# Kernel optimization log

Hardware: AMD Instinct MI355X
Metric: run time of the kernel (lower is better)

## Reference

```python
import jax, jax.numpy as jnp
import numpy as np
from functools import partial

N_NODES = 100000
N_EDGES = 3200000
F_IN, H1, H2, C_OUT = 128, 64, 32, 2


def setup_inputs() -> dict:
    key = jax.random.key(0)
    ks = jax.random.split(key, 8)
    x = jax.random.normal(ks[0], (N_NODES, F_IN), dtype=jnp.float32)
    edge_index = jax.random.randint(ks[1], (2, N_EDGES), 0, N_NODES, dtype=jnp.int64)
    def glorot(k, fan_in, fan_out):
        s = jnp.sqrt(6.0 / (fan_in + fan_out))
        return jax.random.uniform(k, (fan_in, fan_out), jnp.float32, -s, s)
    return {
        "x": x,
        "edge_index": edge_index,
        "W1": glorot(ks[2], F_IN, H1), "b1": jnp.zeros((H1,), jnp.float32),
        "W2": glorot(ks[3], H1, H2),   "b2": jnp.zeros((H2,), jnp.float32),
        "W3": glorot(ks[4], H2, C_OUT), "b3": jnp.zeros((C_OUT,), jnp.float32),
    }


def _gcn_norm(edge_index, num_nodes):
    # add self-loops, compute symmetric normalization D^{-1/2} (A+I) D^{-1/2}
    loop = jnp.arange(num_nodes, dtype=edge_index.dtype)
    src = jnp.concatenate([edge_index[0], loop])
    dst = jnp.concatenate([edge_index[1], loop])
    deg = jax.ops.segment_sum(jnp.ones_like(dst, dtype=jnp.float32), dst,
                              num_segments=num_nodes)
    dinv = jax.lax.rsqrt(deg)  # deg >= 1 because of self-loops
    norm = dinv[src] * dinv[dst]  # [E + N]
    return src, dst, norm


def _gcn_conv(x, W, b, src, dst, norm, num_nodes):
    # PyG GCNConv: linear transform, then normalized scatter-aggregate, then bias
    xw = x @ W                                   # [N, F_out]
    msg = xw[src] * norm[:, None]                # [E+N, F_out] gather + scale
    out = jax.ops.segment_sum(msg, dst, num_segments=num_nodes)
    return out + b


def reference(x, edge_index, W1, b1, W2, b2, W3, b3):
    n = x.shape[0]
    src, dst, norm = _gcn_norm(edge_index, n)
    h = jax.nn.relu(_gcn_conv(x, W1, b1, src, dst, norm, n))
    # dropout is identity in eval mode
    h = jax.nn.relu(_gcn_conv(h, W2, b2, src, dst, norm, n))
    h = _gcn_conv(h, W3, b3, src, dst, norm, n)
    return jax.nn.log_softmax(h, axis=1)
```

## Files before the change

kernel.cpp:

```cpp
#include <hip/hip_runtime.h>
#include <hip/hip_bf16.h>
#include <math.h>

constexpr int N = 100000;
constexpr int E = 3200000;
constexpr int FIN = 128, H1 = 64, H2 = 32, COUT = 2;

constexpr int BUK_SHIFT = 6;
constexpr int BUK_NODES = 64;
constexpr int NBUK = (N + BUK_NODES - 1) / BUK_NODES;
constexpr int CAP = 2560;
constexpr int SEG_SHIFT = 14;
constexpr int NSEG = 7;
constexpr int KEYS = BUK_NODES * NSEG;
constexpr int RP_STR = BUK_NODES + 1;

constexpr int MS_TPB = 1024;
constexpr int MS_EPT = 24;
constexpr int CHUNK = MS_TPB * MS_EPT;
constexpr int MS_WGS = (E + CHUNK - 1) / CHUNK;

__global__ void k_initcur(int* __restrict__ gcursor) {
    int i = blockIdx.x * blockDim.x + threadIdx.x;
    if (i < NBUK) gcursor[i] = i * CAP;
}

__global__ __launch_bounds__(MS_TPB)
void k_mslice(const int* __restrict__ src, const int* __restrict__ dst,
              int* __restrict__ gcursor, unsigned* __restrict__ ebuf) {
    __shared__ int cnt[NBUK];
    __shared__ int base[NBUK];
    const int t = threadIdx.x;
    for (int i = t; i < NBUK; i += MS_TPB) cnt[i] = 0;
    __syncthreads();
    const int e0 = blockIdx.x * CHUNK;

    int rb[MS_EPT];
    unsigned rv[MS_EPT];
#pragma unroll
    for (int j = 0; j < MS_EPT; ++j) {
        int e = e0 + j * MS_TPB + t;
        if (e < E) {
            int d = dst[e];
            int b = d >> BUK_SHIFT;
            rb[j] = b;
            rv[j] = (unsigned)src[e] | ((unsigned)(d & (BUK_NODES - 1)) << 17);
            atomicAdd(&cnt[b], 1);
        } else {
            rb[j] = -1; rv[j] = 0;
        }
    }
    __syncthreads();
    for (int i = t; i < NBUK; i += MS_TPB) {
        int c = cnt[i];
        base[i] = c ? atomicAdd(&gcursor[i], c) : 0;
    }
    __syncthreads();
    for (int i = t; i < NBUK; i += MS_TPB) cnt[i] = 0;
    __syncthreads();
#pragma unroll
    for (int j = 0; j < MS_EPT; ++j) {
        int b = rb[j];
        if (b >= 0) {
            int r = atomicAdd(&cnt[b], 1);
            int p = base[b] + r;
            if (p < (b + 1) * CAP) ebuf[p] = rv[j];
        }
    }
}

__global__ __launch_bounds__(256)
void k_build(const int* __restrict__ gcursor, unsigned* __restrict__ ebuf,
             int* __restrict__ rp, float* __restrict__ dinv) {
    __shared__ unsigned ent[CAP];
    __shared__ int cnt[512];
    __shared__ int sa[512];
    __shared__ int sb[512];
    __shared__ int cur[512];
    const int b = blockIdx.x;
    const int t = threadIdx.x;
    int fill = gcursor[b] - b * CAP;
    if (fill > CAP) fill = CAP;
    const int gbase = b * CAP;

    cnt[t] = 0; cnt[t + 256] = 0;
    __syncthreads();
    for (int j = t; j < fill; j += 256) {
        unsigned v = ebuf[gbase + j];
        ent[j] = v;
        int key = (int)(v >> 17) * NSEG + (int)((v & 0x1FFFFu) >> SEG_SHIFT);
        atomicAdd(&cnt[key], 1);
    }
    __syncthreads();
    sa[t] = cnt[t]; sa[t + 256] = cnt[t + 256];
    __syncthreads();
    int* pin = sa; int* pout = sb;
    for (int off = 1; off < 512; off <<= 1) {
        pout[t]       = pin[t]       + ((t >= off)       ? pin[t - off]       : 0);
        pout[t + 256] = pin[t + 256] + ((t + 256 >= off) ? pin[t + 256 - off] : 0);
        __syncthreads();
        int* tmp = pin; pin = pout; pout = tmp;
    }
    {
        int ex0 = pin[t] - cnt[t];
        int ex1 = pin[t + 256] - cnt[t + 256];
        cur[t] = gbase + ex0;
        cur[t + 256] = gbase + ex1;
        if (t < KEYS && (t % NSEG) == 0)
            rp[b * RP_STR + t / NSEG] = gbase + ex0;
        int k2 = t + 256;
        if (k2 < KEYS && (k2 % NSEG) == 0)
            rp[b * RP_STR + k2 / NSEG] = gbase + ex1;
        if (t == 0) rp[b * RP_STR + BUK_NODES] = gbase + fill;
    }
    if (t < BUK_NODES) {
        int deg = 0;
#pragma unroll
        for (int s = 0; s < NSEG; ++s) deg += cnt[t * NSEG + s];
        int node = (b << BUK_SHIFT) + t;
        if (node < N) dinv[node] = rsqrtf((float)deg + 1.0f);
    }
    __syncthreads();
    for (int j = t; j < fill; j += 256) {
        unsigned v = ent[j];
        int key = (int)(v >> 17) * NSEG + (int)((v & 0x1FFFFu) >> SEG_SHIFT);
        int p = atomicAdd(&cur[key], 1);
        ebuf[p] = v & 0x1FFFFu;
    }
}

template<int FI, int FO>
__global__ __launch_bounds__(256)
void k_gemm_tile_bf(const float* __restrict__ h, const float* __restrict__ Wg,
                    const float* __restrict__ dinv, __hip_bfloat16* __restrict__ y) {
    constexpr int TX  = FO / 4;
    constexpr int TY  = 256 / TX;
    constexpr int RPT = 64 / TY;
    constexpr int XS  = 68;
    constexpr int KQ  = FI / 4;

    __shared__ float xsT[FI][XS];

    const int tid = threadIdx.x;
    const int tx = tid % TX;
    const int ty = tid / TX;
    const int row0 = blockIdx.x * 64;

    for (int idx = tid; idx < 64 * KQ; idx += 256) {
        int g   = idx / 8;
        int rlo = idx % 8;
        int k4  = g % KQ;
        int rhi = g / KQ;
        int r   = rlo + 8 * rhi;
        int row = row0 + r;
        float4 v = make_float4(0.f, 0.f, 0.f, 0.f);
        if (row < N) v = *(const float4*)(h + (size_t)row * FI + 4 * k4);
        xsT[4 * k4 + 0][r] = v.x;
        xsT[4 * k4 + 1][r] = v.y;
        xsT[4 * k4 + 2][r] = v.z;
        xsT[4 * k4 + 3][r] = v.w;
    }
    __syncthreads();

    float acc[RPT][4];
#pragma unroll
    for (int i = 0; i < RPT; ++i)
#pragma unroll
        for (int c = 0; c < 4; ++c) acc[i][c] = 0.0f;

#pragma unroll 4
    for (int k = 0; k < FI; ++k) {
        const float4 wv = *(const float4*)(Wg + (size_t)k * FO + 4 * tx);
        float xv[RPT];
        if constexpr (RPT == 4) {
            float4 t = *(const float4*)&xsT[k][4 * ty];
            xv[0] = t.x; xv[1] = t.y; xv[2] = t.z; xv[3] = t.w;
        } else {
            float2 t = *(const float2*)&xsT[k][2 * ty];
            xv[0] = t.x; xv[1] = t.y;
        }
#pragma unroll
        for (int i = 0; i < RPT; ++i) {
            acc[i][0] = fmaf(xv[i], wv.x, acc[i][0]);
            acc[i][1] = fmaf(xv[i], wv.y, acc[i][1]);
            acc[i][2] = fmaf(xv[i], wv.z, acc[i][2]);
            acc[i][3] = fmaf(xv[i], wv.w, acc[i][3]);
        }
    }

#pragma unroll
    for (int i = 0; i < RPT; ++i) {
        int row = row0 + ty * RPT + i;
        if (row >= N) continue;
        float di = dinv[row];
        auto cvt = [](float f) -> unsigned short {
            __hip_bfloat16 b = __float2bfloat16(f);
            return *reinterpret_cast<unsigned short*>(&b);
        };
        ushort4 pk;
        pk.x = cvt(di * acc[i][0]);
        pk.y = cvt(di * acc[i][1]);
        pk.z = cvt(di * acc[i][2]);
        pk.w = cvt(di * acc[i][3]);
        *(ushort4*)&y[(size_t)row * FO + 4 * tx] = pk;
    }
}

template<int FI, int FO, int ROWS>
__global__ __launch_bounds__(FO * ROWS)
void k_gemm_scale(const float* __restrict__ h, const float* __restrict__ W,
                  const float* __restrict__ dinv, float* __restrict__ y) {
    __shared__ float xs[ROWS][FI];
    const int j = threadIdx.x;
    const int r = threadIdx.y;
    const int row0 = blockIdx.x * ROWS;
    const int tid = r * FO + j;
    constexpr int NT = FO * ROWS;
    for (int t = tid; t < ROWS * FI; t += NT) {
        int rr = t / FI, kk = t % FI;
        int row = row0 + rr;
        xs[rr][kk] = (row < N) ? h[(size_t)row * FI + kk] : 0.0f;
    }
    __syncthreads();
    const int row = row0 + r;
    if (row >= N) return;
    float acc = 0.0f;
#pragma unroll
    for (int k = 0; k < FI; ++k)
        acc = fmaf(xs[r][k], W[k * FO + j], acc);
    y[(size_t)row * FO + j] = dinv[row] * acc;
}

template<int F, bool RELU>
__global__ __launch_bounds__(256)
void k_agg_v(const int* __restrict__ rp, const unsigned* __restrict__ csr,
             const __hip_bfloat16* __restrict__ y, const float* __restrict__ dinv,
             const float* __restrict__ b, float* __restrict__ out) {
    constexpr int LPN = F / 8;
    constexpr int NPB = 256 / LPN;
    const int fp = threadIdx.x;
    const int n = blockIdx.x * NPB + threadIdx.y;
    if (n >= N) return;
    const uint4* yq = (const uint4*)y;

    float acc[8];
    auto unpk = [](unsigned w, float& lo, float& hi) {
        lo = __uint_as_float(w << 16);
        hi = __uint_as_float(w & 0xffff0000u);
    };
    auto accum = [&](uint4 v) {
        float l0, h0, l1, h1, l2, h2, l3, h3;
        unpk(v.x, l0, h0); unpk(v.y, l1, h1);
        unpk(v.z, l2, h2); unpk(v.w, l3, h3);
        acc[0] += l0; acc[1] += h0; acc[2] += l1; acc[3] += h1;
        acc[4] += l2; acc[5] += h2; acc[6] += l3; acc[7] += h3;
    };

    {
        uint4 v = yq[(size_t)n * LPN + fp];
        float l0, h0, l1, h1, l2, h2, l3, h3;
        unpk(v.x, l0, h0); unpk(v.y, l1, h1);
        unpk(v.z, l2, h2); unpk(v.w, l3, h3);
        acc[0] = l0; acc[1] = h0; acc[2] = l1; acc[3] = h1;
        acc[4] = l2; acc[5] = h2; acc[6] = l3; acc[7] = h3;
    }

    const int rb = (n >> BUK_SHIFT) * RP_STR + (n & (BUK_NODES - 1));
    int j = rp[rb];
    const int j1 = rp[rb + 1];
    for (; j + 8 <= j1; j += 8) {
        int s0 = (int)csr[j],     s1 = (int)csr[j + 1], s2 = (int)csr[j + 2], s3 = (int)csr[j + 3];
        int s4 = (int)csr[j + 4], s5 = (int)csr[j + 5], s6 = (int)csr[j + 6], s7 = (int)csr[j + 7];
        uint4 v0 = yq[(size_t)s0 * LPN + fp], v1 = yq[(size_t)s1 * LPN + fp];
        uint4 v2 = yq[(size_t)s2 * LPN + fp], v3 = yq[(size_t)s3 * LPN + fp];
        uint4 v4 = yq[(size_t)s4 * LPN + fp], v5 = yq[(size_t)s5 * LPN + fp];
        uint4 v6 = yq[(size_t)s6 * LPN + fp], v7 = yq[(size_t)s7 * LPN + fp];
        accum(v0); accum(v1); accum(v2); accum(v3);
        accum(v4); accum(v5); accum(v6); accum(v7);
    }
    for (; j < j1; ++j) {
        uint4 v = yq[(size_t)(int)csr[j] * LPN + fp];
        accum(v);
    }

    const float di = dinv[n];
    float4 o0, o1;
    o0.x = fmaf(di, acc[0], b[8 * fp + 0]);
    o0.y = fmaf(di, acc[1], b[8 * fp + 1]);
    o0.z = fmaf(di, acc[2], b[8 * fp + 2]);
    o0.w = fmaf(di, acc[3], b[8 * fp + 3]);
    o1.x = fmaf(di, acc[4], b[8 * fp + 4]);
    o1.y = fmaf(di, acc[5], b[8 * fp + 5]);
    o1.z = fmaf(di, acc[6], b[8 * fp + 6]);
    o1.w = fmaf(di, acc[7], b[8 * fp + 7]);
    if (RELU) {
        o0.x = fmaxf(o0.x, 0.f); o0.y = fmaxf(o0.y, 0.f);
        o0.z = fmaxf(o0.z, 0.f); o0.w = fmaxf(o0.w, 0.f);
        o1.x = fmaxf(o1.x, 0.f); o1.y = fmaxf(o1.y, 0.f);
        o1.z = fmaxf(o1.z, 0.f); o1.w = fmaxf(o1.w, 0.f);
    }
    float* op = out + (size_t)n * F + 8 * fp;
    *(float4*)op = o0;
    *(float4*)(op + 4) = o1;
}

__global__ __launch_bounds__(256)
void k_final(const int* __restrict__ rp, const unsigned* __restrict__ csr,
             const float* __restrict__ y, const float* __restrict__ dinv,
             const float* __restrict__ bias, float* __restrict__ out) {
    const int c = threadIdx.x;
    const int n = blockIdx.x * 128 + threadIdx.y;
    float z = 0.0f;
    if (n < N) {
        const int rb = (n >> BUK_SHIFT) * RP_STR + (n & (BUK_NODES - 1));
        int j = rp[rb];
        const int j1 = rp[rb + 1];
        float acc = y[2 * n + c];
        for (; j + 4 <= j1; j += 4) {
            int s0 = (int)csr[j], s1 = (int)csr[j + 1], s2 = (int)csr[j + 2], s3 = (int)csr[j + 3];
            float a0 = y[2 * s0 + c], a1 = y[2 * s1 + c];
            float a2 = y[2 * s2 + c], a3 = y[2 * s3 + c];
            acc += (a0 + a1) + (a2 + a3);
        }
        for (; j < j1; ++j) acc += y[2 * (int)csr[j] + c];
        z = fmaf(dinv[n], acc, bias[c]);
    }
    float zo = __shfl_xor(z, 1);
    if (n < N) {
        float m = fmaxf(z, zo);
        float lse = m + logf(expf(z - m) + expf(zo - m));
        out[2 * n + c] = z - lse;
    }
}

extern "C" void kernel_launch(void* const* d_in, const int* in_sizes, int n_in,
                              void* d_out, int out_size, void* d_ws, size_t ws_size,
                              hipStream_t stream) {
    const float* x   = (const float*)d_in[0];
    const int*   ei  = (const int*)d_in[1];
    const float* W1  = (const float*)d_in[2];
    const float* b1  = (const float*)d_in[3];
    const float* W2  = (const float*)d_in[4];
    const float* b2  = (const float*)d_in[5];
    const float* W3  = (const float*)d_in[6];
    const float* b3  = (const float*)d_in[7];
    float* out = (float*)d_out;

    const int* src = ei;
    const int* dst = ei + E;

    char* p = (char*)d_ws;
    float*    dinv    = (float*)p;    p += (size_t)N * 4;
    int*      gcursor = (int*)p;      p += (size_t)NBUK * 4;
    int*      rp      = (int*)p;      p += (size_t)NBUK * RP_STR * 4;
    unsigned* ebuf    = (unsigned*)p; p += (size_t)NBUK * CAP * 4;
    char*     bufA    = p;            p += (size_t)N * 64 * 4;
    char*     bufB    = p;            p += (size_t)N * 64 * 4;

    __hip_bfloat16* y1 = (__hip_bfloat16*)bufA;
    float*          h1 = (float*)bufB;
    __hip_bfloat16* y2 = (__hip_bfloat16*)bufA;
    float*          h2 = (float*)(bufA + (size_t)N * H2 * 2);
    float*          y3 = (float*)bufB;

    k_initcur<<<(NBUK + 255) / 256, 256, 0, stream>>>(gcursor);
    k_mslice <<<MS_WGS, MS_TPB, 0, stream>>>(src, dst, gcursor, ebuf);
    k_build  <<<NBUK, 256, 0, stream>>>(gcursor, ebuf, rp, dinv);

    k_gemm_tile_bf<FIN, H1><<<(N + 63) / 64, 256, 0, stream>>>(x, W1, dinv, y1);
    k_agg_v<H1, true><<<(N + 31) / 32, dim3(8, 32), 0, stream>>>(rp, ebuf, y1, dinv, b1, h1);

    k_gemm_tile_bf<H1, H2><<<(N + 63) / 64, 256, 0, stream>>>(h1, W2, dinv, y2);
    k_agg_v<H2, true><<<(N + 63) / 64, dim3(4, 64), 0, stream>>>(rp, ebuf, y2, dinv, b2, h2);

    k_gemm_scale<H2, COUT, 128><<<(N + 127) / 128, dim3(COUT, 128), 0, stream>>>(h2, W3, dinv, y3);
    k_final<<<(N + 127) / 128, dim3(2, 128), 0, stream>>>(rp, ebuf, y3, dinv, b3, out);
}
```

Measured before the change: 380.5 us.

## Slice bf16 features into 16-wide planes and aggregate one plane per pass

```diff
diff --git a/kernel.cpp b/kernel.cpp
--- a/kernel.cpp
+++ b/kernel.cpp
@@ -19,6 +19,8 @@
 constexpr int MS_EPT = 24;
 constexpr int CHUNK = MS_TPB * MS_EPT;
 constexpr int MS_WGS = (E + CHUNK - 1) / CHUNK;
+
+typedef float f32x4 __attribute__((ext_vector_type(4)));
 
 __global__ void k_initcur(int* __restrict__ gcursor) {
     int i = blockIdx.x * blockDim.x + threadIdx.x;
@@ -133,6 +135,7 @@
 __global__ __launch_bounds__(256)
 void k_gemm_tile_bf(const float* __restrict__ h, const float* __restrict__ Wg,
                     const float* __restrict__ dinv, __hip_bfloat16* __restrict__ y) {
+    static_assert(FO % 16 == 0, "slice width 16");
     constexpr int TX  = FO / 4;
     constexpr int TY  = 256 / TX;
     constexpr int RPT = 64 / TY;
@@ -188,6 +191,8 @@
         }
     }
 
+    const int p  = (4 * tx) / 16;
+    const int fo = (4 * tx) % 16;
 #pragma unroll
     for (int i = 0; i < RPT; ++i) {
         int row = row0 + ty * RPT + i;
@@ -202,7 +207,7 @@
         pk.y = cvt(di * acc[i][1]);
         pk.z = cvt(di * acc[i][2]);
         pk.w = cvt(di * acc[i][3]);
-        *(ushort4*)&y[(size_t)row * FO + 4 * tx] = pk;
+        *(ushort4*)&y[((size_t)p * N + row) * 16 + fo] = pk;
     }
 }
 
@@ -233,75 +238,86 @@
 
 template<int F, bool RELU>
 __global__ __launch_bounds__(256)
-void k_agg_v(const int* __restrict__ rp, const unsigned* __restrict__ csr,
-             const __hip_bfloat16* __restrict__ y, const float* __restrict__ dinv,
-             const float* __restrict__ b, float* __restrict__ out) {
-    constexpr int LPN = F / 8;
-    constexpr int NPB = 256 / LPN;
+void k_agg_pw(const int* __restrict__ rp, const unsigned* __restrict__ csr,
+              const __hip_bfloat16* __restrict__ y, const float* __restrict__ dinv,
+              const float* __restrict__ b, float* __restrict__ out) {
+    constexpr int NPASS = F / 16;
+    constexpr int QPP   = 2;
+    constexpr int NPB   = 256 / QPP;
     const int fp = threadIdx.x;
     const int n = blockIdx.x * NPB + threadIdx.y;
     if (n >= N) return;
     const uint4* yq = (const uint4*)y;
 
-    float acc[8];
+    const int rb = (n >> BUK_SHIFT) * RP_STR + (n & (BUK_NODES - 1));
+    const int j0 = rp[rb];
+    const int j1 = rp[rb + 1];
+    const float di = dinv[n];
+
     auto unpk = [](unsigned w, float& lo, float& hi) {
         lo = __uint_as_float(w << 16);
         hi = __uint_as_float(w & 0xffff0000u);
     };
-    auto accum = [&](uint4 v) {
-        float l0, h0, l1, h1, l2, h2, l3, h3;
-        unpk(v.x, l0, h0); unpk(v.y, l1, h1);
-        unpk(v.z, l2, h2); unpk(v.w, l3, h3);
-        acc[0] += l0; acc[1] += h0; acc[2] += l1; acc[3] += h1;
-        acc[4] += l2; acc[5] += h2; acc[6] += l3; acc[7] += h3;
-    };
-
-    {
-        uint4 v = yq[(size_t)n * LPN + fp];
-        float l0, h0, l1, h1, l2, h2, l3, h3;
-        unpk(v.x, l0, h0); unpk(v.y, l1, h1);
-        unpk(v.z, l2, h2); unpk(v.w, l3, h3);
-        acc[0] = l0; acc[1] = h0; acc[2] = l1; acc[3] = h1;
-        acc[4] = l2; acc[5] = h2; acc[6] = l3; acc[7] = h3;
-    }
-
-    const int rb = (n >> BUK_SHIFT) * RP_STR + (n & (BUK_NODES - 1));
-    int j = rp[rb];
-    const int j1 = rp[rb + 1];
-    for (; j + 8 <= j1; j += 8) {
-        int s0 = (int)csr[j],     s1 = (int)csr[j + 1], s2 = (int)csr[j + 2], s3 = (int)csr[j + 3];
-        int s4 = (int)csr[j + 4], s5 = (int)csr[j + 5], s6 = (int)csr[j + 6], s7 = (int)csr[j + 7];
-        uint4 v0 = yq[(size_t)s0 * LPN + fp], v1 = yq[(size_t)s1 * LPN + fp];
-        uint4 v2 = yq[(size_t)s2 * LPN + fp], v3 = yq[(size_t)s3 * LPN + fp];
-        uint4 v4 = yq[(size_t)s4 * LPN + fp], v5 = yq[(size_t)s5 * LPN + fp];
-        uint4 v6 = yq[(size_t)s6 * LPN + fp], v7 = yq[(size_t)s7 * LPN + fp];
-        accum(v0); accum(v1); accum(v2); accum(v3);
-        accum(v4); accum(v5); accum(v6); accum(v7);
-    }
-    for (; j < j1; ++j) {
-        uint4 v = yq[(size_t)(int)csr[j] * LPN + fp];
-        accum(v);
-    }
-
-    const float di = dinv[n];
-    float4 o0, o1;
-    o0.x = fmaf(di, acc[0], b[8 * fp + 0]);
-    o0.y = fmaf(di, acc[1], b[8 * fp + 1]);
-    o0.z = fmaf(di, acc[2], b[8 * fp + 2]);
-    o0.w = fmaf(di, acc[3], b[8 * fp + 3]);
-    o1.x = fmaf(di, acc[4], b[8 * fp + 4]);
-    o1.y = fmaf(di, acc[5], b[8 * fp + 5]);
-    o1.z = fmaf(di, acc[6], b[8 * fp + 6]);
-    o1.w = fmaf(di, acc[7], b[8 * fp + 7]);
-    if (RELU) {
-        o0.x = fmaxf(o0.x, 0.f); o0.y = fmaxf(o0.y, 0.f);
-        o0.z = fmaxf(o0.z, 0.f); o0.w = fmaxf(o0.w, 0.f);
-        o1.x = fmaxf(o1.x, 0.f); o1.y = fmaxf(o1.y, 0.f);
-        o1.z = fmaxf(o1.z, 0.f); o1.w = fmaxf(o1.w, 0.f);
-    }
-    float* op = out + (size_t)n * F + 8 * fp;
-    *(float4*)op = o0;
-    *(float4*)(op + 4) = o1;
+
+#pragma unroll 1
+    for (int p = 0; p < NPASS; ++p) {
+        const size_t sbase = (size_t)p * N * QPP + fp;
+        float acc[8];
+        {
+            uint4 v = yq[sbase + (size_t)n * QPP];
+            unpk(v.x, acc[0], acc[1]); unpk(v.y, acc[2], acc[3]);
+            unpk(v.z, acc[4], acc[5]); unpk(v.w, acc[6], acc[7]);
+        }
+        auto accum = [&](uint4 v) {
+            float l0, h0, l1, h1, l2, h2, l3, h3;
+            unpk(v.x, l0, h0); unpk(v.y, l1, h1);
+            unpk(v.z, l2, h2); unpk(v.w, l3, h3);
+            acc[0] += l0; acc[1] += h0; acc[2] += l1; acc[3] += h1;
+            acc[4] += l2; acc[5] += h2; acc[6] += l3; acc[7] += h3;
+        };
+
+        int j = j0;
+        for (; j + 8 <= j1; j += 8) {
+            int s0 = (int)__builtin_nontemporal_load(&csr[j]);
+            int s1 = (int)__builtin_nontemporal_load(&csr[j + 1]);
+            int s2 = (int)__builtin_nontemporal_load(&csr[j + 2]);
+            int s3 = (int)__builtin_nontemporal_load(&csr[j + 3]);
+            int s4 = (int)__builtin_nontemporal_load(&csr[j + 4]);
+            int s5 = (int)__builtin_nontemporal_load(&csr[j + 5]);
+            int s6 = (int)__builtin_nontemporal_load(&csr[j + 6]);
+            int s7 = (int)__builtin_nontemporal_load(&csr[j + 7]);
+            uint4 v0 = yq[sbase + (size_t)s0 * QPP], v1 = yq[sbase + (size_t)s1 * QPP];
+            uint4 v2 = yq[sbase + (size_t)s2 * QPP], v3 = yq[sbase + (size_t)s3 * QPP];
+            uint4 v4 = yq[sbase + (size_t)s4 * QPP], v5 = yq[sbase + (size_t)s5 * QPP];
+            uint4 v6 = yq[sbase + (size_t)s6 * QPP], v7 = yq[sbase + (size_t)s7 * QPP];
+            accum(v0); accum(v1); accum(v2); accum(v3);
+            accum(v4); accum(v5); accum(v6); accum(v7);
+        }
+        for (; j < j1; ++j) {
+            int s = (int)__builtin_nontemporal_load(&csr[j]);
+            accum(yq[sbase + (size_t)s * QPP]);
+        }
+
+        const float* bp = b + p * 16 + 8 * fp;
+        f32x4 o0, o1;
+        o0.x = fmaf(di, acc[0], bp[0]);
+        o0.y = fmaf(di, acc[1], bp[1]);
+        o0.z = fmaf(di, acc[2], bp[2]);
+        o0.w = fmaf(di, acc[3], bp[3]);
+        o1.x = fmaf(di, acc[4], bp[4]);
+        o1.y = fmaf(di, acc[5], bp[5]);
+        o1.z = fmaf(di, acc[6], bp[6]);
+        o1.w = fmaf(di, acc[7], bp[7]);
+        if (RELU) {
+            o0.x = fmaxf(o0.x, 0.f); o0.y = fmaxf(o0.y, 0.f);
+            o0.z = fmaxf(o0.z, 0.f); o0.w = fmaxf(o0.w, 0.f);
+            o1.x = fmaxf(o1.x, 0.f); o1.y = fmaxf(o1.y, 0.f);
+            o1.z = fmaxf(o1.z, 0.f); o1.w = fmaxf(o1.w, 0.f);
+        }
+        float* op = out + (size_t)n * F + p * 16 + 8 * fp;
+        __builtin_nontemporal_store(o0, (f32x4*)op);
+        __builtin_nontemporal_store(o1, (f32x4*)(op + 4));
+    }
 }
 
 __global__ __launch_bounds__(256)
@@ -368,10 +384,10 @@
     k_build  <<<NBUK, 256, 0, stream>>>(gcursor, ebuf, rp, dinv);
 
     k_gemm_tile_bf<FIN, H1><<<(N + 63) / 64, 256, 0, stream>>>(x, W1, dinv, y1);
-    k_agg_v<H1, true><<<(N + 31) / 32, dim3(8, 32), 0, stream>>>(rp, ebuf, y1, dinv, b1, h1);
+    k_agg_pw<H1, true><<<(N + 127) / 128, dim3(2, 128), 0, stream>>>(rp, ebuf, y1, dinv, b1, h1);
 
     k_gemm_tile_bf<H1, H2><<<(N + 63) / 64, 256, 0, stream>>>(h1, W2, dinv, y2);
-    k_agg_v<H2, true><<<(N + 63) / 64, dim3(4, 64), 0, stream>>>(rp, ebuf, y2, dinv, b2, h2);
+    k_agg_pw<H2, true><<<(N + 127) / 128, dim3(2, 128), 0, stream>>>(rp, ebuf, y2, dinv, b2, h2);
 
     k_gemm_scale<H2, COUT, 128><<<(N + 127) / 128, dim3(COUT, 128), 0, stream>>>(h2, W3, dinv, y3);
     k_final<<<(N + 127) / 128, dim3(2, 128), 0, stream>>>(rp, ebuf, y3, dinv, b3, out);
```

New measurement: 520.2 us. 36.7% more time.

## Use split-bf16 MFMA for dense GCN layer GEMMs

Applied to the files above, without the earlier changes.

```diff
diff --git a/kernel.cpp b/kernel.cpp
--- a/kernel.cpp
+++ b/kernel.cpp
@@ -19,6 +19,10 @@
 constexpr int MS_EPT = 24;
 constexpr int CHUNK = MS_TPB * MS_EPT;
 constexpr int MS_WGS = (E + CHUNK - 1) / CHUNK;
+
+typedef float f32x4 __attribute__((ext_vector_type(4)));
+typedef short bf16x8 __attribute__((ext_vector_type(8)));
+typedef short s16x4 __attribute__((ext_vector_type(4)));
 
 __global__ void k_initcur(int* __restrict__ gcursor) {
     int i = blockIdx.x * blockDim.x + threadIdx.x;
@@ -131,78 +135,97 @@
 
 template<int FI, int FO>
 __global__ __launch_bounds__(256)
-void k_gemm_tile_bf(const float* __restrict__ h, const float* __restrict__ Wg,
-                    const float* __restrict__ dinv, __hip_bfloat16* __restrict__ y) {
-    constexpr int TX  = FO / 4;
-    constexpr int TY  = 256 / TX;
-    constexpr int RPT = 64 / TY;
-    constexpr int XS  = 68;
-    constexpr int KQ  = FI / 4;
-
-    __shared__ float xsT[FI][XS];
+void k_gemm_mfma(const float* __restrict__ h, const float* __restrict__ Wg,
+                 const float* __restrict__ dinv, __hip_bfloat16* __restrict__ y) {
+    constexpr int KH  = (FI > 64) ? 64 : FI;
+    constexpr int NPH = FI / KH;
+    constexpr int KP  = KH + 8;
+    constexpr int NCT = FO / 16;
+
+    __shared__ short xh[64 * KP];
+    __shared__ short xl[64 * KP];
+    __shared__ short wh[FO * KP];
+    __shared__ short wl[FO * KP];
 
     const int tid = threadIdx.x;
-    const int tx = tid % TX;
-    const int ty = tid / TX;
+    const int w   = tid >> 6;
+    const int l   = tid & 63;
+    const int lm  = l & 15;
+    const int lg  = l >> 4;
     const int row0 = blockIdx.x * 64;
 
-    for (int idx = tid; idx < 64 * KQ; idx += 256) {
-        int g   = idx / 8;
-        int rlo = idx % 8;
-        int k4  = g % KQ;
-        int rhi = g / KQ;
-        int r   = rlo + 8 * rhi;
-        int row = row0 + r;
-        float4 v = make_float4(0.f, 0.f, 0.f, 0.f);
-        if (row < N) v = *(const float4*)(h + (size_t)row * FI + 4 * k4);
-        xsT[4 * k4 + 0][r] = v.x;
-        xsT[4 * k4 + 1][r] = v.y;
-        xsT[4 * k4 + 2][r] = v.z;
-        xsT[4 * k4 + 3][r] = v.w;
-    }
-    __syncthreads();
-
-    float acc[RPT][4];
-#pragma unroll
-    for (int i = 0; i < RPT; ++i)
-#pragma unroll
-        for (int c = 0; c < 4; ++c) acc[i][c] = 0.0f;
-
-#pragma unroll 4
-    for (int k = 0; k < FI; ++k) {
-        const float4 wv = *(const float4*)(Wg + (size_t)k * FO + 4 * tx);
-        float xv[RPT];
-        if constexpr (RPT == 4) {
-            float4 t = *(const float4*)&xsT[k][4 * ty];
-            xv[0] = t.x; xv[1] = t.y; xv[2] = t.z; xv[3] = t.w;
-        } else {
-            float2 t = *(const float2*)&xsT[k][2 * ty];
-            xv[0] = t.x; xv[1] = t.y;
-        }
-#pragma unroll
-        for (int i = 0; i < RPT; ++i) {
-            acc[i][0] = fmaf(xv[i], wv.x, acc[i][0]);
-            acc[i][1] = fmaf(xv[i], wv.y, acc[i][1]);
-            acc[i][2] = fmaf(xv[i], wv.z, acc[i][2]);
-            acc[i][3] = fmaf(xv[i], wv.w, acc[i][3]);
-        }
-    }
-
-#pragma unroll
-    for (int i = 0; i < RPT; ++i) {
-        int row = row0 + ty * RPT + i;
-        if (row >= N) continue;
-        float di = dinv[row];
-        auto cvt = [](float f) -> unsigned short {
-            __hip_bfloat16 b = __float2bfloat16(f);
-            return *reinterpret_cast<unsigned short*>(&b);
-        };
-        ushort4 pk;
-        pk.x = cvt(di * acc[i][0]);
-        pk.y = cvt(di * acc[i][1]);
-        pk.z = cvt(di * acc[i][2]);
-        pk.w = cvt(di * acc[i][3]);
-        *(ushort4*)&y[(size_t)row * FO + 4 * tx] = pk;
+    auto cvt_hi = [](float f) -> short {
+        __hip_bfloat16 b = __float2bfloat16(f);
+        return *reinterpret_cast<short*>(&b);
+    };
+    auto bf2f = [](short s) -> float {
+        return __uint_as_float(((unsigned)(unsigned short)s) << 16);
+    };
+
+    f32x4 acc[NCT];
+#pragma unroll
+    for (int ct = 0; ct < NCT; ++ct) acc[ct] = f32x4{0.f, 0.f, 0.f, 0.f};
+
+    for (int ph = 0; ph < NPH; ++ph) {
+        if (ph) __syncthreads();
+        for (int idx = tid; idx < 64 * KH / 4; idx += 256) {
+            int r  = idx / (KH / 4);
+            int k4 = idx % (KH / 4);
+            int row = row0 + r;
+            float4 v = make_float4(0.f, 0.f, 0.f, 0.f);
+            if (row < N) v = *(const float4*)(h + (size_t)row * FI + ph * KH + 4 * k4);
+            float vv[4] = {v.x, v.y, v.z, v.w};
+            s16x4 ph4, pl4;
+#pragma unroll
+            for (int i = 0; i < 4; ++i) {
+                short hi = cvt_hi(vv[i]);
+                ph4[i] = hi;
+                pl4[i] = cvt_hi(vv[i] - bf2f(hi));
+            }
+            *(s16x4*)&xh[r * KP + 4 * k4] = ph4;
+            *(s16x4*)&xl[r * KP + 4 * k4] = pl4;
+        }
+        for (int idx = tid; idx < KH * FO; idx += 256) {
+            int k = idx / FO;
+            int c = idx % FO;
+            float wv = Wg[(size_t)(ph * KH + k) * FO + c];
+            short hi = cvt_hi(wv);
+            wh[c * KP + k] = hi;
+            wl[c * KP + k] = cvt_hi(wv - bf2f(hi));
+        }
+        __syncthreads();
+
+#pragma unroll
+        for (int k0 = 0; k0 < KH; k0 += 32) {
+            const int ka = (16 * w + lm) * KP + k0 + 8 * lg;
+            bf16x8 ah = *(const bf16x8*)&xh[ka];
+            bf16x8 al = *(const bf16x8*)&xl[ka];
+#pragma unroll
+            for (int ct = 0; ct < NCT; ++ct) {
+                const int kb = (16 * ct + lm) * KP + k0 + 8 * lg;
+                bf16x8 bh = *(const bf16x8*)&wh[kb];
+                bf16x8 bl = *(const bf16x8*)&wl[kb];
+                acc[ct] = __builtin_amdgcn_mfma_f32_16x16x32_bf16(ah, bh, acc[ct], 0, 0, 0);
+                acc[ct] = __builtin_amdgcn_mfma_f32_16x16x32_bf16(ah, bl, acc[ct], 0, 0, 0);
+                acc[ct] = __builtin_amdgcn_mfma_f32_16x16x32_bf16(al, bh, acc[ct], 0, 0, 0);
+            }
+        }
+    }
+
+    float di[4];
+#pragma unroll
+    for (int i = 0; i < 4; ++i) {
+        int row = row0 + 16 * w + 4 * lg + i;
+        di[i] = (row < N) ? dinv[row] : 0.f;
+    }
+#pragma unroll
+    for (int ct = 0; ct < NCT; ++ct) {
+#pragma unroll
+        for (int i = 0; i < 4; ++i) {
+            int row = row0 + 16 * w + 4 * lg + i;
+            if (row < N)
+                y[(size_t)row * FO + 16 * ct + lm] = __float2bfloat16(di[i] * acc[ct][i]);
+        }
     }
 }
 
@@ -367,10 +390,10 @@
     k_mslice <<<MS_WGS, MS_TPB, 0, stream>>>(src, dst, gcursor, ebuf);
     k_build  <<<NBUK, 256, 0, stream>>>(gcursor, ebuf, rp, dinv);
 
-    k_gemm_tile_bf<FIN, H1><<<(N + 63) / 64, 256, 0, stream>>>(x, W1, dinv, y1);
+    k_gemm_mfma<FIN, H1><<<(N + 63) / 64, 256, 0, stream>>>(x, W1, dinv, y1);
     k_agg_v<H1, true><<<(N + 31) / 32, dim3(8, 32), 0, stream>>>(rp, ebuf, y1, dinv, b1, h1);
 
-    k_gemm_tile_bf<H1, H2><<<(N + 63) / 64, 256, 0, stream>>>(h1, W2, dinv, y2);
+    k_gemm_mfma<H1, H2><<<(N + 63) / 64, 256, 0, stream>>>(h1, W2, dinv, y2);
     k_agg_v<H2, true><<<(N + 63) / 64, dim3(4, 64), 0, stream>>>(rp, ebuf, y2, dinv, b2, h2);
 
     k_gemm_scale<H2, COUT, 128><<<(N + 127) / 128, dim3(COUT, 128), 0, stream>>>(h2, W3, dinv, y3);
```

New measurement: 369.0 us (median of 2 runs). 3.0% less time.
